# Optimization experiments

Measured on AMD Instinct MI355X. Metric: run time of the kernel, lower is better.

Reference implementation:

```python
import jax, jax.numpy as jnp
import numpy as np

HEAD = 32  # HEAD_SIZE
B, T, C = 8, 1024, 768
LAYER_ID, N_LAYER = 2, 12


def wkv7(r, w, k, v, a, b):
    # RWKV7 linear recurrence (matches the custom CUDA 'attn' kernel math):
    #   S = S * exp(-exp(w)) + (S @ a) b^T + v k^T ;  y = S @ r
    Bb, Tt, Cc = r.shape
    H, N = Cc // HEAD, HEAD
    rs = lambda z: jnp.moveaxis(z.reshape(Bb, Tt, H, N), 1, 0)  # [T,B,H,N]
    rT, kT, vT, aT, bT = rs(r), rs(k), rs(v), rs(a), rs(b)
    wT = rs(jnp.exp(-jnp.exp(w)))  # decay in (0,1)
    def step(S, inp):
        rt, wt, kt, vt, at, bt = inp  # each [B,H,N]
        sa = jnp.einsum('bhij,bhj->bhi', S, at)
        S = S * wt[:, :, None, :] + sa[..., None] * bt[:, :, None, :] + vt[..., None] * kt[:, :, None, :]
        return S, jnp.einsum('bhij,bhj->bhi', S, rt)
    S0 = jnp.zeros((Bb, H, N, N), r.dtype)
    _, y = jax.lax.scan(step, S0, (rT, wT, kT, vT, aT, bT))
    return jnp.moveaxis(y, 0, 1).reshape(Bb, Tt, Cc)


def setup_inputs() -> dict:
    key = jax.random.key(0)
    ks = iter(jax.random.split(key, 64))
    def rn(shape, s=0.02):
        return (jax.random.normal(next(ks), shape, jnp.float32) * s)
    def un(shape, lim):
        return jax.random.uniform(next(ks), shape, jnp.float32, -lim, lim)
    H, N = C // HEAD, HEAD
    r10 = 1.0 - LAYER_ID / N_LAYER          # ratio_1_to_almost0
    r01 = LAYER_ID / (N_LAYER - 1)          # ratio_0_to_1
    ddd = (np.arange(C, dtype=np.float64) / C).reshape(1, 1, C)
    f32 = lambda z: jnp.asarray(z, jnp.float32)
    time_maa_x = f32(1.0 - ddd ** (0.6 * r10 ** 0.9))
    time_maa_rg = f32(1.0 - ddd ** (0.2 * r10))
    time_maa_wa = f32(1.0 - ddd ** (0.9 * r10))
    time_maa_k = f32(1.0 - (ddd ** (0.9 * r10) + 0.4 * r01))
    time_maa_v = f32(1.0 - (ddd ** (0.4 * r10) + 0.6 * r01))
    ds = -7.0 + 5.0 * (np.arange(C, dtype=np.float64) / (C - 1)) ** (0.85 + r01 ** 0.5)
    time_decay = f32(ds.reshape(1, 1, C) + 0.5)
    inp = {
        'x': jax.random.normal(next(ks), (B, T, C), jnp.float32),
        'v1': jax.random.normal(next(ks), (B, T, C), jnp.float32),
        'time_maa_x': time_maa_x, 'time_maa_rg': time_maa_rg, 'time_maa_wa': time_maa_wa,
        'time_maa_k': time_maa_k, 'time_maa_v': time_maa_v,
        'time_decay': time_decay,
        'time_faaaa': rn((1, 1, H, N), 0.05),
        'time_aaaaa': rn((1, 1, C), 0.05),
        'time_maa_w1': rn((C, 28 * 4)), 'time_maa_w2': rn((4, 28, C), 0.05),
        'time_decay_w1': rn((C, 64)), 'time_decay_w2': rn((64, C), 0.05),
        'time_aaa_w1': rn((C, 24)), 'time_aaa_w2': rn((24, C), 0.05),
        'time_kkk_w1': rn((C, 24)), 'time_kkk_w2': rn((24, C), 0.05),
        'gate_w1': rn((C, 120)), 'gate_w2': rn((120, C), 0.05),
        'ma_w1': rn((C, 24)), 'ma_w2': rn((24, C), 0.05), 'time_misc_a': rn((1, 1, C), 0.05),
        'mk_w1': rn((C, 24)), 'mk_w2': rn((24, C), 0.05), 'time_misc_k': rn((1, 1, C), 0.05),
        'mv_w1': rn((C, 24)), 'mv_w2': rn((24, C), 0.05), 'time_misc_v': 1.0 + rn((1, 1, C), 0.05),
        'Wr': un((C, C), 0.5 / C ** 0.5), 'Wk': un((C, C), 0.05 / C ** 0.5),
        'Wv': un((C, C), 0.5 / C ** 0.5), 'Wo': rn((C, C), 0.02),
        'ln_w': jnp.ones((C,), jnp.float32), 'ln_b': jnp.zeros((C,), jnp.float32),
    }
    return inp


def reference(x, v1, time_maa_x, time_maa_rg, time_maa_wa, time_maa_k, time_maa_v,
              time_decay, time_faaaa, time_aaaaa, time_maa_w1, time_maa_w2,
              time_decay_w1, time_decay_w2, time_aaa_w1, time_aaa_w2,
              time_kkk_w1, time_kkk_w2, gate_w1, gate_w2, ma_w1, ma_w2, time_misc_a,
              mk_w1, mk_w2, time_misc_k, mv_w1, mv_w2, time_misc_v,
              Wr, Wk, Wv, Wo, ln_w, ln_b):
    Bb, Tt, Cc = x.shape
    H, N = Cc // HEAD, HEAD
    # token shift: xx[t] = x[t-1] - x[t], with x[-1] = 0
    xsh = jnp.concatenate([jnp.zeros_like(x[:, :1]), x[:, :-1]], axis=1)
    xx = xsh - x
    xxx = x + xx * time_maa_x
    tm = jnp.tanh(xxx @ time_maa_w1).reshape(Bb, Tt, 4, -1)      # [B,T,4,28]
    mix = jnp.einsum('btfd,fdc->fbtc', tm, time_maa_w2)          # [4,B,T,C]
    xrg = x + xx * (time_maa_rg + mix[0])
    xwa = x + xx * (time_maa_wa + mix[1])
    xk = x + xx * (time_maa_k + mix[2])
    xv = x + xx * (time_maa_v + mix[3])
    r = xrg @ Wr
    w = -jax.nn.softplus(-(time_decay + jnp.tanh(xwa @ time_decay_w1) @ time_decay_w2)) - 0.5
    k = xk @ Wk
    v = xv @ Wv
    v = v + (v1 - v) * jax.nn.sigmoid(time_misc_v + xv @ mv_w1 @ mv_w2)
    g = jax.nn.sigmoid(xrg @ gate_w1) @ gate_w2
    kk = k + jnp.tanh(xk @ time_kkk_w1) @ time_kkk_w2
    kk4 = kk.reshape(Bb, Tt, H, N)
    nrm = jnp.maximum(jnp.sqrt(jnp.sum(kk4 * kk4, axis=-1, keepdims=True)), 1e-12)
    kk = (kk4 / nrm).reshape(Bb, Tt, Cc)
    a = jax.nn.sigmoid(time_aaaaa + xwa @ time_aaa_w1 @ time_aaa_w2)
    ma = jax.nn.sigmoid(time_misc_a + xwa @ ma_w1 @ ma_w2)
    k = k * ma + k * a * (1.0 - ma)
    mk = jax.nn.sigmoid(time_misc_k + xk @ mk_w1 @ mk_w2)
    k = k * jnp.exp(jnp.minimum(w * mk, 0.0))
    y = wkv7(r, w, k, v, -kk, kk * a)
    # GroupNorm(n_head groups) over each token, eps=6.4e-5
    yg = y.reshape(Bb, Tt, H, N)
    mu = jnp.mean(yg, axis=-1, keepdims=True)
    var = jnp.var(yg, axis=-1, keepdims=True)
    yn = (yg - mu) * jax.lax.rsqrt(var + 6.4e-05)
    yn = yn * ln_w.reshape(H, N) + ln_b.reshape(H, N)
    # per-head bonus term
    bonus = (jnp.sum(r.reshape(Bb, Tt, H, N) * k.reshape(Bb, Tt, H, N) * time_faaaa,
                     axis=-1, keepdims=True) * v.reshape(Bb, Tt, H, N))
    y = yn.reshape(Bb, Tt, Cc) + bonus.reshape(Bb, Tt, Cc)
    out = (y * g) @ Wo
    return (out, v1)
```

## Files before the change

kernel.cpp:

```cpp
#include <hip/hip_runtime.h>
#include <hip/hip_bf16.h>
#include <math.h>

#define Bdim 8
#define Tdim 1024
#define Cdim 768
#define Hdim 24
#define Ndim 32
#define BTdim (Bdim*Tdim)

typedef __attribute__((ext_vector_type(8))) short bf16x8;
typedef __attribute__((ext_vector_type(4))) float f32x4;
typedef __hip_bfloat16 bf16;

__device__ __forceinline__ float sigm(float x){ return 1.f/(1.f+expf(-x)); }
__device__ __forceinline__ float softplusf(float x){ return fmaxf(x,0.f) + log1pf(expf(-fabsf(x))); }
__device__ __forceinline__ float bf2f(bf16 v){ return __bfloat162float(v); }
__device__ __forceinline__ float us2f(unsigned short s){ return __builtin_bit_cast(float, (unsigned)s<<16); }

template<int CTRL>
__device__ __forceinline__ float dpp_add(float x){
  int xi = __builtin_bit_cast(int, x);
  int yi = __builtin_amdgcn_mov_dpp(xi, CTRL, 0xF, 0xF, true);
  return x + __builtin_bit_cast(float, yi);
}
__device__ __forceinline__ float red32(float x){
  x = dpp_add<0xB1>(x);
  x = dpp_add<0x4E>(x);
  x = dpp_add<0x141>(x);
  x = dpp_add<0x140>(x);
  x += __shfl_xor(x, 16);
  return x;
}
__device__ __forceinline__ float red16(float x){
  x = dpp_add<0xB1>(x);
  x = dpp_add<0x4E>(x);
  x = dpp_add<0x141>(x);
  x = dpp_add<0x140>(x);
  return x;
}

#define GLDS16(gp, lp) __builtin_amdgcn_global_load_lds((const __attribute__((address_space(1))) void*)(gp), (__attribute__((address_space(3))) void*)(lp), 16, 0, 0)

__global__ void k1_shift(const float* __restrict__ x, const float* __restrict__ maa_x,
                         float* __restrict__ xx, bf16* __restrict__ xxx) {
  int idx = blockIdx.x*256 + threadIdx.x;
  if (idx >= BTdim*Cdim) return;
  int c = idx % Cdim; int row = idx / Cdim; int t = row % Tdim;
  float xv = x[idx];
  float xp = (t==0) ? 0.f : x[idx - Cdim];
  float d = xp - xv;
  xx[idx] = d;
  xxx[idx] = __float2bfloat16(xv + d*maa_x[c]);
}

__global__ __launch_bounds__(256) void kconvW(const float* __restrict__ W0, const float* __restrict__ W1,
    const float* __restrict__ W2, const float* __restrict__ W3,
    bf16* __restrict__ T0, bf16* __restrict__ T1, bf16* __restrict__ T2, bf16* __restrict__ T3) {
  const float* Wsrc[4] = {W0,W1,W2,W3};
  bf16* Tdst[4] = {T0,T1,T2,T3};
  const float* W = Wsrc[blockIdx.z];
  bf16* T = Tdst[blockIdx.z];
  __shared__ float tile[32][33];
  int bx = blockIdx.x*32, by = blockIdx.y*32;
  int tx = threadIdx.x & 31, ty = threadIdx.x >> 5;
  #pragma unroll
  for (int q=0;q<32;q+=8) tile[ty+q][tx] = W[(size_t)(by+ty+q)*Cdim + bx+tx];
  __syncthreads();
  #pragma unroll
  for (int q=0;q<32;q+=8) T[(size_t)(bx+ty+q)*Cdim + by+tx] = __float2bfloat16(tile[tx][ty+q]);
}

__global__ __launch_bounds__(256) void kprep(const float* __restrict__ dw1, const float* __restrict__ aaa_w1,
    const float* __restrict__ ma_w1, const float* __restrict__ kkk_w1, const float* __restrict__ mk_w1,
    const float* __restrict__ mv_w1, const float* __restrict__ gate_w1, const float* __restrict__ maa_w1,
    const float* __restrict__ dw2, const float* __restrict__ aaa_w2, const float* __restrict__ ma_w2,
    const float* __restrict__ kkk_w2, const float* __restrict__ mk_w2, const float* __restrict__ mv_w2,
    const float* __restrict__ gate_w2,
    bf16* __restrict__ PWwa, bf16* __restrict__ PWk, bf16* __restrict__ PWv,
    bf16* __restrict__ PWrg, bf16* __restrict__ PWmaa,
    bf16* __restrict__ W2wa, bf16* __restrict__ W2k, bf16* __restrict__ W2v, bf16* __restrict__ W2g){
  int idx = blockIdx.x*256 + threadIdx.x;
  if (idx < 491520) {
    int buf = idx / 98304, rem = idx - buf*98304;
    int n = rem / 768, kk = rem - n*768;
    float val = 0.f;
    bf16* dst;
    switch(buf){
      case 0: dst=PWwa; if(n<64) val=dw1[(size_t)kk*64+n]; else if(n<88) val=aaa_w1[(size_t)kk*24+(n-64)]; else if(n<112) val=ma_w1[(size_t)kk*24+(n-88)]; break;
      case 1: dst=PWk;  if(n<24) val=kkk_w1[(size_t)kk*24+n]; else if(n<48) val=mk_w1[(size_t)kk*24+(n-24)]; break;
      case 2: dst=PWv;  if(n<24) val=mv_w1[(size_t)kk*24+n]; break;
      case 3: dst=PWrg; if(n<120) val=gate_w1[(size_t)kk*120+n]; break;
      default: dst=PWmaa; if(n<112) val=maa_w1[(size_t)kk*112+n]; break;
    }
    dst[rem] = __float2bfloat16(val);
    return;
  }
  int i = idx - 491520;
  if (i < 294912){
    int n=i>>7, q=i&127, seg=n/768, c=n-seg*768;
    float val=0.f;
    if (seg==0){ if(q<64) val=dw2[(size_t)q*768+c]; }
    else if (seg==1){ if(q>=64&&q<88) val=aaa_w2[(size_t)(q-64)*768+c]; }
    else { if(q>=88&&q<112) val=ma_w2[(size_t)(q-88)*768+c]; }
    W2wa[i]=__float2bfloat16(val); return;
  }
  i -= 294912;
  if (i < 98304){
    int n=i>>6, q=i&63, seg=n/768, c=n-seg*768;
    float val=0.f;
    if (seg==0){ if(q<24) val=kkk_w2[(size_t)q*768+c]; }
    else { if(q>=24&&q<48) val=mk_w2[(size_t)(q-24)*768+c]; }
    W2k[i]=__float2bfloat16(val); return;
  }
  i -= 98304;
  if (i < 24576){
    int c=i>>5, q=i&31;
    float val = (q<24) ? mv_w2[(size_t)q*768+c] : 0.f;
    W2v[i]=__float2bfloat16(val); return;
  }
  i -= 24576;
  if (i < 98304){
    int c=i>>7, q=i&127;
    float val = (q<120) ? gate_w2[(size_t)q*768+c] : 0.f;
    W2g[i]=__float2bfloat16(val);
  }
}

__global__ __launch_bounds__(256) void gemm_mfma(const bf16* __restrict__ A,
    const bf16* __restrict__ Bt, float* __restrict__ C, int M, int N, int K) {
  __shared__ unsigned short As[128*32];
  __shared__ unsigned short Bs[128*32];
  const int bm = blockIdx.y*128, bn = blockIdx.x*128;
  const int tid = threadIdx.x, lane = tid&63, w = tid>>6;
  const int wr = w>>1, wc = w&1;
  const int lr = lane&15, kg = lane>>4;
  f32x4 zero = {0.f,0.f,0.f,0.f};
  f32x4 acc[4][4];
  #pragma unroll
  for (int m=0;m<4;m++)
    #pragma unroll
    for (int n=0;n<4;n++) acc[m][n]=zero;
  const size_t rowA = (size_t)(bm + w*32 + (lane>>2))*K + (lane&3)*8;
  const size_t rowB = (size_t)(bn + w*32 + (lane>>2))*K + (lane&3)*8;
  unsigned short* lA = As + w*32*32;
  unsigned short* lB = Bs + w*32*32;
  for (int k0=0; k0<K; k0+=32){
    GLDS16(A + rowA + k0,                 lA);
    GLDS16(A + rowA + k0 + (size_t)16*K,  lA + 512);
    GLDS16(Bt + rowB + k0,                lB);
    GLDS16(Bt + rowB + k0 + (size_t)16*K, lB + 512);
    __syncthreads();
    bf16x8 af[4], bfr[4];
    #pragma unroll
    for (int m=0;m<4;m++) af[m]  = *(const bf16x8*)(void*)(As + (wr*64+m*16+lr)*32 + kg*8);
    #pragma unroll
    for (int n=0;n<4;n++) bfr[n] = *(const bf16x8*)(void*)(Bs + (wc*64+n*16+lr)*32 + kg*8);
    #pragma unroll
    for (int m=0;m<4;m++)
      #pragma unroll
      for (int n=0;n<4;n++)
        acc[m][n] = __builtin_amdgcn_mfma_f32_16x16x32_bf16(af[m], bfr[n], acc[m][n], 0,0,0);
    __syncthreads();
  }
  #pragma unroll
  for (int m=0;m<4;m++)
    #pragma unroll
    for (int n=0;n<4;n++){
      size_t r0 = (size_t)(bm + wr*64 + m*16 + kg*4);
      int cc = bn + wc*64 + n*16 + lr;
      #pragma unroll
      for (int q=0;q<4;q++)
        C[(r0+q)*N + cc] = acc[m][n][q];
    }
}

struct G3 {
  const bf16* A[3];
  const bf16* Bt[3];
  bf16* C[3];
};
__global__ __launch_bounds__(256) void gemm_big3(G3 p, int N, int K) {
  const int z = blockIdx.z;
  const bf16* __restrict__ A  = p.A[z];
  const bf16* __restrict__ Bt = p.Bt[z];
  bf16* __restrict__ C = p.C[z];
  __shared__ unsigned short As[128*32];
  __shared__ unsigned short Bs[128*32];
  const int bm = blockIdx.y*128, bn = blockIdx.x*128;
  const int tid = threadIdx.x, lane = tid&63, w = tid>>6;
  const int wr = w>>1, wc = w&1;
  const int lr = lane&15, kg = lane>>4;
  f32x4 zero = {0.f,0.f,0.f,0.f};
  f32x4 acc[4][4];
  #pragma unroll
  for (int m=0;m<4;m++)
    #pragma unroll
    for (int n=0;n<4;n++) acc[m][n]=zero;
  const size_t rowA = (size_t)(bm + w*32 + (lane>>2))*K + (lane&3)*8;
  const size_t rowB = (size_t)(bn + w*32 + (lane>>2))*K + (lane&3)*8;
  unsigned short* lA = As + w*32*32;
  unsigned short* lB = Bs + w*32*32;
  for (int k0=0; k0<K; k0+=32){
    GLDS16(A + rowA + k0,                 lA);
    GLDS16(A + rowA + k0 + (size_t)16*K,  lA + 512);
    GLDS16(Bt + rowB + k0,                lB);
    GLDS16(Bt + rowB + k0 + (size_t)16*K, lB + 512);
    __syncthreads();
    bf16x8 af[4], bfr[4];
    #pragma unroll
    for (int m=0;m<4;m++) af[m]  = *(const bf16x8*)(void*)(As + (wr*64+m*16+lr)*32 + kg*8);
    #pragma unroll
    for (int n=0;n<4;n++) bfr[n] = *(const bf16x8*)(void*)(Bs + (wc*64+n*16+lr)*32 + kg*8);
    #pragma unroll
    for (int m=0;m<4;m++)
      #pragma unroll
      for (int n=0;n<4;n++)
        acc[m][n] = __builtin_amdgcn_mfma_f32_16x16x32_bf16(af[m], bfr[n], acc[m][n], 0,0,0);
    __syncthreads();
  }
  #pragma unroll
  for (int m=0;m<4;m++)
    #pragma unroll
    for (int n=0;n<4;n++){
      size_t r0 = (size_t)(bm + wr*64 + m*16 + kg*4);
      int cc = bn + wc*64 + n*16 + lr;
      #pragma unroll
      for (int q=0;q<4;q++)
        C[(r0+q)*N + cc] = __float2bfloat16(acc[m][n][q]);
    }
}

__global__ __launch_bounds__(256) void gemm_tm(const bf16* __restrict__ A,
    const bf16* __restrict__ Bt, float* __restrict__ C, int K) {
  __shared__ unsigned short As[128*32];
  __shared__ unsigned short Bs[128*32];
  const int bm = blockIdx.y*128;
  const int tid = threadIdx.x, lane = tid&63, w = tid>>6;
  const int wr = w>>1, wc = w&1;
  const int lr = lane&15, kg = lane>>4;
  f32x4 zero = {0.f,0.f,0.f,0.f};
  f32x4 acc[4][4];
  #pragma unroll
  for (int m=0;m<4;m++)
    #pragma unroll
    for (int n=0;n<4;n++) acc[m][n]=zero;
  const size_t rowA = (size_t)(bm + w*32 + (lane>>2))*K + (lane&3)*8;
  const size_t rowB = (size_t)(w*32 + (lane>>2))*K + (lane&3)*8;
  unsigned short* lA = As + w*32*32;
  unsigned short* lB = Bs + w*32*32;
  for (int k0=0; k0<K; k0+=32){
    GLDS16(A + rowA + k0,                 lA);
    GLDS16(A + rowA + k0 + (size_t)16*K,  lA + 512);
    GLDS16(Bt + rowB + k0,                lB);
    GLDS16(Bt + rowB + k0 + (size_t)16*K, lB + 512);
    __syncthreads();
    bf16x8 af[4], bfr[4];
    #pragma unroll
    for (int m=0;m<4;m++) af[m]  = *(const bf16x8*)(void*)(As + (wr*64+m*16+lr)*32 + kg*8);
    #pragma unroll
    for (int n=0;n<4;n++) bfr[n] = *(const bf16x8*)(void*)(Bs + (wc*64+n*16+lr)*32 + kg*8);
    #pragma unroll
    for (int m=0;m<4;m++)
      #pragma unroll
      for (int n=0;n<4;n++)
        acc[m][n] = __builtin_amdgcn_mfma_f32_16x16x32_bf16(af[m], bfr[n], acc[m][n], 0,0,0);
    __syncthreads();
  }
  #pragma unroll
  for (int m=0;m<4;m++)
    #pragma unroll
    for (int n=0;n<4;n++){
      size_t r0 = (size_t)(bm + wr*64 + m*16 + kg*4);
      int cc = wc*64 + n*16 + lr;
      if (cc < 112){
        #pragma unroll
        for (int q=0;q<4;q++)
          C[(r0+q)*112 + cc] = tanhf(acc[m][n][q]);
      }
    }
}

struct S1P {
  const bf16* A[4];
  const bf16* Bt[4];
  bf16* C[4];
  int Ntrue[4];
  int Nalloc[4];
  int act[4];
};
__global__ __launch_bounds__(256) void gemm_s1(S1P p, int K) {
  const int z = blockIdx.z;
  const bf16* __restrict__ A  = p.A[z];
  const bf16* __restrict__ Bt = p.Bt[z];
  bf16* __restrict__ C = p.C[z];
  const int Ntrue = p.Ntrue[z], Nalloc = p.Nalloc[z], act = p.act[z];
  __shared__ unsigned short As[128*32];
  __shared__ unsigned short Bs[128*32];
  const int bm = blockIdx.y*128;
  const int tid = threadIdx.x, lane = tid&63, w = tid>>6;
  const int wr = w>>1, wc = w&1;
  const int lr = lane&15, kg = lane>>4;
  f32x4 zero = {0.f,0.f,0.f,0.f};
  f32x4 acc[4][4];
  #pragma unroll
  for (int m=0;m<4;m++)
    #pragma unroll
    for (int n=0;n<4;n++) acc[m][n]=zero;
  const size_t rowA = (size_t)(bm + w*32 + (lane>>2))*K + (lane&3)*8;
  const size_t rowB = (size_t)(w*32 + (lane>>2))*K + (lane&3)*8;
  unsigned short* lA = As + w*32*32;
  unsigned short* lB = Bs + w*32*32;
  for (int k0=0; k0<K; k0+=32){
    GLDS16(A + rowA + k0,                 lA);
    GLDS16(A + rowA + k0 + (size_t)16*K,  lA + 512);
    GLDS16(Bt + rowB + k0,                lB);
    GLDS16(Bt + rowB + k0 + (size_t)16*K, lB + 512);
    __syncthreads();
    bf16x8 af[4], bfr[4];
    #pragma unroll
    for (int m=0;m<4;m++) af[m]  = *(const bf16x8*)(void*)(As + (wr*64+m*16+lr)*32 + kg*8);
    #pragma unroll
    for (int n=0;n<4;n++) bfr[n] = *(const bf16x8*)(void*)(Bs + (wc*64+n*16+lr)*32 + kg*8);
    #pragma unroll
    for (int m=0;m<4;m++)
      #pragma unroll
      for (int n=0;n<4;n++)
        acc[m][n] = __builtin_amdgcn_mfma_f32_16x16x32_bf16(af[m], bfr[n], acc[m][n], 0,0,0);
    __syncthreads();
  }
  #pragma unroll
  for (int m=0;m<4;m++)
    #pragma unroll
    for (int n=0;n<4;n++){
      size_t r0 = (size_t)(bm + wr*64 + m*16 + kg*4);
      int cc = wc*64 + n*16 + lr;
      if (cc < Nalloc){
        #pragma unroll
        for (int q=0;q<4;q++){
          float val = acc[m][n][q];
          if      (act==1){ if (cc<64) val = tanhf(val); }
          else if (act==2){ if (cc<24) val = tanhf(val); }
          else if (act==3){ val = sigm(val); }
          if (cc >= Ntrue) val = 0.f;
          C[(r0+q)*Nalloc + cc] = __float2bfloat16(val);
        }
      }
    }
}

struct Z4 {
  const bf16* A[4];
  const bf16* Bt[4];
  bf16* C[4];
  int N[4];
  int K[4];
};
__global__ __launch_bounds__(256) void gemm_z(Z4 p) {
  const int z = blockIdx.z;
  const int N = p.N[z], K = p.K[z];
  const int bn = blockIdx.x*128;
  if (bn >= N) return;
  const bf16* __restrict__ A  = p.A[z];
  const bf16* __restrict__ Bt = p.Bt[z];
  bf16* __restrict__ C = p.C[z];
  __shared__ unsigned short As[128*32];
  __shared__ unsigned short Bs[128*32];
  const int bm = blockIdx.y*128;
  const int tid = threadIdx.x, lane = tid&63, w = tid>>6;
  const int wr = w>>1, wc = w&1;
  const int lr = lane&15, kg = lane>>4;
  f32x4 zero = {0.f,0.f,0.f,0.f};
  f32x4 acc[4][4];
  #pragma unroll
  for (int m=0;m<4;m++)
    #pragma unroll
    for (int n=0;n<4;n++) acc[m][n]=zero;
  const size_t rowA = (size_t)(bm + w*32 + (lane>>2))*K + (lane&3)*8;
  const size_t rowB = (size_t)(bn + w*32 + (lane>>2))*K + (lane&3)*8;
  unsigned short* lA = As + w*32*32;
  unsigned short* lB = Bs + w*32*32;
  for (int k0=0; k0<K; k0+=32){
    GLDS16(A + rowA + k0,                 lA);
    GLDS16(A + rowA + k0 + (size_t)16*K,  lA + 512);
    GLDS16(Bt + rowB + k0,                lB);
    GLDS16(Bt + rowB + k0 + (size_t)16*K, lB + 512);
    __syncthreads();
    bf16x8 af[4], bfr[4];
    #pragma unroll
    for (int m=0;m<4;m++) af[m]  = *(const bf16x8*)(void*)(As + (wr*64+m*16+lr)*32 + kg*8);
    #pragma unroll
    for (int n=0;n<4;n++) bfr[n] = *(const bf16x8*)(void*)(Bs + (wc*64+n*16+lr)*32 + kg*8);
    #pragma unroll
    for (int m=0;m<4;m++)
      #pragma unroll
      for (int n=0;n<4;n++)
        acc[m][n] = __builtin_amdgcn_mfma_f32_16x16x32_bf16(af[m], bfr[n], acc[m][n], 0,0,0);
    __syncthreads();
  }
  #pragma unroll
  for (int m=0;m<4;m++)
    #pragma unroll
    for (int n=0;n<4;n++){
      size_t r0 = (size_t)(bm + wr*64 + m*16 + kg*4);
      int cc = bn + wc*64 + n*16 + lr;
      #pragma unroll
      for (int q=0;q<4;q++)
        C[(r0+q)*N + cc] = __float2bfloat16(acc[m][n][q]);
    }
}

__global__ __launch_bounds__(256) void k2_mix(const float* __restrict__ x, const float* __restrict__ xx,
    const float* __restrict__ tm, const float* __restrict__ w2,
    const float* __restrict__ mrg, const float* __restrict__ mwa,
    const float* __restrict__ mk_, const float* __restrict__ mv_,
    bf16* __restrict__ xrg, bf16* __restrict__ xwa, bf16* __restrict__ xk, bf16* __restrict__ xv) {
  const int row0 = blockIdx.x*8, tid = threadIdx.x;
  __shared__ float stm[8][112];
  for (int idx=tid; idx<8*112; idx+=256){
    int rr=idx/112, q=idx-rr*112;
    stm[rr][q]=tm[(size_t)(row0+rr)*112+q];
  }
  __syncthreads();
  for (int c=tid;c<Cdim;c+=256){
    float x8[8], d8[8];
    #pragma unroll
    for (int rr=0;rr<8;rr++){
      size_t i=(size_t)(row0+rr)*Cdim+c;
      x8[rr]=x[i]; d8[rr]=xx[i];
    }
    float mrgc=mrg[c], mwac=mwa[c], mkc=mk_[c], mvc=mv_[c];
    float m0[8]={},m1[8]={},m2[8]={},m3[8]={};
    #pragma unroll 4
    for (int d=0; d<28; d++){
      float w0=w2[(size_t)(d)*Cdim + c];
      float w1=w2[(size_t)(28+d)*Cdim + c];
      float w2v=w2[(size_t)(56+d)*Cdim + c];
      float w3=w2[(size_t)(84+d)*Cdim + c];
      #pragma unroll
      for (int rr=0;rr<8;rr++){
        m0[rr]+=stm[rr][d]*w0; m1[rr]+=stm[rr][28+d]*w1;
        m2[rr]+=stm[rr][56+d]*w2v; m3[rr]+=stm[rr][84+d]*w3;
      }
    }
    #pragma unroll
    for (int rr=0;rr<8;rr++){
      size_t i=(size_t)(row0+rr)*Cdim+c;
      xrg[i]=__float2bfloat16(x8[rr] + d8[rr]*(mrgc+m0[rr]));
      xwa[i]=__float2bfloat16(x8[rr] + d8[rr]*(mwac+m1[rr]));
      xk[i] =__float2bfloat16(x8[rr] + d8[rr]*(mkc+m2[rr]));
      xv[i] =__float2bfloat16(x8[rr] + d8[rr]*(mvc+m3[rr]));
    }
  }
}

__global__ __launch_bounds__(256) void k5_fuse(
    const bf16* __restrict__ zwa, const bf16* __restrict__ zk, const bf16* __restrict__ zv,
    const bf16* __restrict__ rbf, const bf16* __restrict__ kbf, bf16* __restrict__ vbf,
    const float* __restrict__ td, const float* __restrict__ aaaaa,
    const float* __restrict__ misc_a, const float* __restrict__ misc_k, const float* __restrict__ misc_v,
    const float* __restrict__ v1,
    float* __restrict__ wexp, unsigned short* __restrict__ rkab) {
  const int row = blockIdx.x, tid = threadIdx.x;
  #pragma unroll
  for (int it=0;it<3;it++){
    const int c = tid + it*256;
    const size_t i = (size_t)row*Cdim + c;
    float kraw = bf2f(kbf[i]);
    float v0   = bf2f(vbf[i]);
    float zd = bf2f(zwa[(size_t)row*2304 + c]);
    float za = bf2f(zwa[(size_t)row*2304 + 768 + c]);
    float zma= bf2f(zwa[(size_t)row*2304 + 1536 + c]);
    float zkk= bf2f(zk[(size_t)row*1536 + c]);
    float zmk= bf2f(zk[(size_t)row*1536 + 768 + c]);
    float zmv= bf2f(zv[i]);
    float w = -softplusf(-(td[c]+zd)) - 0.5f;
    wexp[i] = expf(-expf(w));
    float a  = sigm(aaaaa[c]+za);
    float ma = sigm(misc_a[c]+zma);
    float mk = sigm(misc_k[c]+zmk);
    float mv = sigm(misc_v[c]+zmv);
    vbf[i] = __float2bfloat16(v0 + (v1[i]-v0)*mv);
    float kf = kraw*(ma + a*(1.f-ma))*expf(fminf(w*mk,0.f));
    float kk = kraw + zkk;
    float ss = red32(kk*kk);
    float kkn = kk * (1.f/fmaxf(sqrtf(ss),1e-12f));
    unsigned rus = (unsigned)__builtin_bit_cast(unsigned short, rbf[i]);
    unsigned kus = (unsigned)__builtin_bit_cast(unsigned short, __float2bfloat16(kf));
    unsigned aus = (unsigned)__builtin_bit_cast(unsigned short, __float2bfloat16(-kkn));
    unsigned bus = (unsigned)__builtin_bit_cast(unsigned short, __float2bfloat16(kkn*a));
    uint2 pk;
    pk.x = rus | (kus<<16);
    pk.y = aus | (bus<<16);
    *(uint2*)&rkab[((size_t)row*Hdim + (c>>5))*128 + (size_t)(c&31)*4] = pk;
  }
}

__global__ __launch_bounds__(64) void k6_wkv(const unsigned short* __restrict__ rkab,
    const float* __restrict__ wd, const unsigned short* __restrict__ vbf, bf16* __restrict__ y) {
  const int lane = threadIdx.x;
  const int bid = blockIdx.x;
  const int head = bid % (Bdim*Hdim);
  const int rq   = bid / (Bdim*Hdim);
  const int bb = head / Hdim, hh = head - bb*Hdim;
  const int i0 = rq*4 + (lane >> 4);
  const int jh = lane & 15;
  __shared__ __align__(16) unsigned short srk[2][16][128];
  __shared__ __align__(16) float sw[2][16][32];
  __shared__ __align__(16) unsigned short sv[2][16][32];
  const size_t wvbase = (size_t)bb*Tdim*Cdim + (size_t)hh*Ndim;
  float S0=0.f, S1=0.f;

  auto rkrow = [&](size_t t){ return (((size_t)bb*Tdim + t)*Hdim + hh)*128; };
  auto STAGE = [&](int c, int buf){
    const size_t tb = (size_t)c*16;
    #pragma unroll
    for (int i=0;i<4;i++)
      GLDS16(rkab + rkrow(tb + i*4 + (lane>>4)) + (size_t)(lane&15)*8, &srk[buf][i*4][0]);
    GLDS16(wd + wvbase + (tb +     (lane>>3))*Cdim + (lane&7)*4, &sw[buf][0][0]);
    GLDS16(wd + wvbase + (tb + 8 + (lane>>3))*Cdim + (lane&7)*4, &sw[buf][8][0]);
    GLDS16(vbf + wvbase + (tb + (lane>>2))*Cdim + (lane&3)*8, &sv[buf][0][0]);
  };

  uint4 nq; float2 nw; unsigned short nv;
  auto LOADT = [&](int buf, int t){
    nq = *(const uint4*)&srk[buf][t][jh*8];
    nw = *(const float2*)&sw[buf][t][jh*2];
    nv = sv[buf][t][i0];
  };

  STAGE(0, 0);
  asm volatile("s_waitcnt vmcnt(0)" ::: "memory");
  LOADT(0, 0);
  int buf = 0;
  const int NCH = Tdim/16;
  for (int c=0; c<NCH; ++c){
    if (c+1 < NCH) STAGE(c+1, buf^1);
    const size_t yb = wvbase + (size_t)c*16*Cdim;
    #pragma unroll
    for (int t=0; t<16; t++){
      const uint4 q = nq;
      const float2 cw = nw;
      const unsigned short cv = nv;
      if (t < 15) {
        LOADT(buf, t+1);
      } else if (c+1 < NCH) {
        asm volatile("s_waitcnt vmcnt(0)" ::: "memory");
        LOADT(buf^1, 0);
      }
      float r0 = __builtin_bit_cast(float, q.x<<16);
      float k0 = __builtin_bit_cast(float, q.x & 0xFFFF0000u);
      float a0 = __builtin_bit_cast(float, q.y<<16);
      float b0 = __builtin_bit_cast(float, q.y & 0xFFFF0000u);
      float r1 = __builtin_bit_cast(float, q.z<<16);
      float k1 = __builtin_bit_cast(float, q.z & 0xFFFF0000u);
      float a1 = __builtin_bit_cast(float, q.w<<16);
      float b1 = __builtin_bit_cast(float, q.w & 0xFFFF0000u);
      const float vl = us2f(cv);
      float sa = S0*a0 + S1*a1;
      sa = red16(sa);
      S0 = S0*cw.x + (sa*b0 + vl*k0);
      S1 = S1*cw.y + (sa*b1 + vl*k1);
      float yv = S0*r0 + S1*r1;
      yv = red16(yv);
      if (jh == 0) y[yb + (size_t)t*Cdim + i0] = __float2bfloat16(yv);
    }
    buf ^= 1;
  }
}

__global__ __launch_bounds__(256) void k7_post(const bf16* __restrict__ y,
    const unsigned short* __restrict__ rkab, const bf16* __restrict__ v,
    const bf16* __restrict__ g, const float* __restrict__ faaaa,
    const float* __restrict__ lnw, const float* __restrict__ lnb,
    bf16* __restrict__ ygate,
    const float4* __restrict__ v1c, float4* __restrict__ outc) {
  const int row = blockIdx.x, tid = threadIdx.x;
  if (tid < 192) outc[(size_t)row*192 + tid] = v1c[(size_t)row*192 + tid];
  #pragma unroll
  for (int it=0; it<3; it++){
    const int c = tid + it*256;
    const size_t i = (size_t)row*Cdim + c;
    float yv = bf2f(y[i]);
    unsigned rk = *(const unsigned*)&rkab[((size_t)row*Hdim + (c>>5))*128 + (size_t)(c&31)*4];
    float rf = __builtin_bit_cast(float, rk<<16);
    float kf = __builtin_bit_cast(float, rk & 0xFFFF0000u);
    float bon = rf*kf*faaaa[c];
    float s  = red32(yv);
    float ss = red32(yv*yv);
    float bn = red32(bon);
    float mu = s*(1.f/Ndim);
    float var = ss*(1.f/Ndim) - mu*mu;
    float rs = rsqrtf(var + 6.4e-5f);
    float yn = (yv-mu)*rs*lnw[c]+lnb[c];
    ygate[i]=__float2bfloat16((yn + bn*bf2f(v[i]))*bf2f(g[i]));
  }
}

extern "C" void kernel_launch(void* const* d_in, const int* in_sizes, int n_in,
                              void* d_out, int out_size, void* d_ws, size_t ws_size,
                              hipStream_t stream) {
  const float* x      = (const float*)d_in[0];
  const float* v1     = (const float*)d_in[1];
  const float* maa_x  = (const float*)d_in[2];
  const float* maa_rg = (const float*)d_in[3];
  const float* maa_wa = (const float*)d_in[4];
  const float* maa_k  = (const float*)d_in[5];
  const float* maa_v  = (const float*)d_in[6];
  const float* time_decay = (const float*)d_in[7];
  const float* faaaa  = (const float*)d_in[8];
  const float* aaaaa  = (const float*)d_in[9];
  const float* maa_w1 = (const float*)d_in[10];
  const float* maa_w2 = (const float*)d_in[11];
  const float* dw1    = (const float*)d_in[12];
  const float* dw2    = (const float*)d_in[13];
  const float* aaa_w1 = (const float*)d_in[14];
  const float* aaa_w2 = (const float*)d_in[15];
  const float* kkk_w1 = (const float*)d_in[16];
  const float* kkk_w2 = (const float*)d_in[17];
  const float* gate_w1= (const float*)d_in[18];
  const float* gate_w2= (const float*)d_in[19];
  const float* ma_w1  = (const float*)d_in[20];
  const float* ma_w2  = (const float*)d_in[21];
  const float* misc_a = (const float*)d_in[22];
  const float* mk_w1  = (const float*)d_in[23];
  const float* mk_w2  = (const float*)d_in[24];
  const float* misc_k = (const float*)d_in[25];
  const float* mv_w1  = (const float*)d_in[26];
  const float* mv_w2  = (const float*)d_in[27];
  const float* misc_v = (const float*)d_in[28];
  const float* Wr     = (const float*)d_in[29];
  const float* Wk     = (const float*)d_in[30];
  const float* Wv     = (const float*)d_in[31];
  const float* Wo     = (const float*)d_in[32];
  const float* lnw    = (const float*)d_in[33];
  const float* lnb    = (const float*)d_in[34];
  float* out = (float*)d_out;

  float* ws = (float*)d_ws;
  const size_t BTC = (size_t)BTdim*Cdim;
  const size_t HB  = BTC/2;
  float* xx    = ws;
  float* wexp  = ws;
  bf16* kb_bf  = (bf16*)(ws + 2*HB);
  bf16* ybuf_bf= (bf16*)(ws + 2*HB);
  bf16* vb_bf  = (bf16*)(ws + 3*HB);
  bf16* xrg_bf = (bf16*)(ws + 4*HB);
  bf16* xwa_bf = xrg_bf + BTC;
  bf16* zwa_bf = (bf16*)(ws + 4*HB);
  bf16* xk_bf  = (bf16*)(ws + 7*HB);
  bf16* xv_bf  = xk_bf + BTC;
  bf16* zk_bf  = (bf16*)(ws + 7*HB);
  bf16* xxx_bf = (bf16*)(ws + 9*HB);
  bf16* zv_bf  = (bf16*)(ws + 9*HB);
  float* tm    = ws + 10*HB;
  bf16* zg_bf  = (bf16*)(ws + 10*HB);
  bf16* hwa_bf = (bf16*)(ws + 11*HB);
  bf16* hk_bf  = hwa_bf + (size_t)BTdim*128;
  bf16* hv_bf  = hk_bf  + (size_t)BTdim*64;
  bf16* hrg_bf = hv_bf  + (size_t)BTdim*32;
  unsigned short* rkab = (unsigned short*)(ws + 12*HB);
  bf16* rb_bf  = (bf16*)(ws + 16*HB);
  bf16* yg_bf  = (bf16*)(ws + 17*HB);
  bf16* Wbase  = (bf16*)(ws + 18*HB);
  bf16* WtR = Wbase;
  bf16* WtK = WtR + 589824;
  bf16* WtV = WtK + 589824;
  bf16* WtO = WtV + 589824;
  bf16* PWwa = WtO + 589824;
  bf16* PWk  = PWwa + 98304;
  bf16* PWv  = PWk  + 98304;
  bf16* PWrg = PWv  + 98304;
  bf16* PWmaa= PWrg + 98304;
  bf16* W2wa = PWmaa + 98304;
  bf16* W2k  = W2wa + 294912;
  bf16* W2v  = W2k  + 98304;
  bf16* W2g  = W2v  + 24576;

  dim3 blk(256);
  kconvW<<<dim3(24,24,4), blk, 0, stream>>>(Wr,Wk,Wv,Wo, WtR,WtK,WtV,WtO);
  kprep<<<dim3(3936), blk, 0, stream>>>(dw1,aaa_w1,ma_w1,kkk_w1,mk_w1,mv_w1,gate_w1,maa_w1,
                                        dw2,aaa_w2,ma_w2,kkk_w2,mk_w2,mv_w2,gate_w2,
                                        PWwa,PWk,PWv,PWrg,PWmaa, W2wa,W2k,W2v,W2g);
  k1_shift<<<dim3((BTdim*Cdim+255)/256), blk, 0, stream>>>(x, maa_x, xx, xxx_bf);
  gemm_tm<<<dim3(1,64), blk, 0, stream>>>(xxx_bf, PWmaa, tm, Cdim);
  k2_mix<<<dim3(BTdim/8), blk, 0, stream>>>(x, xx, tm, maa_w2, maa_rg, maa_wa, maa_k, maa_v,
                                            xrg_bf, xwa_bf, xk_bf, xv_bf);
  {
    S1P p{};
    p.A[0]=xwa_bf; p.Bt[0]=PWwa; p.C[0]=hwa_bf; p.Ntrue[0]=112; p.Nalloc[0]=128; p.act[0]=1;
    p.A[1]=xk_bf;  p.Bt[1]=PWk;  p.C[1]=hk_bf;  p.Ntrue[1]=48;  p.Nalloc[1]=64;  p.act[1]=2;
    p.A[2]=xv_bf;  p.Bt[2]=PWv;  p.C[2]=hv_bf;  p.Ntrue[2]=24;  p.Nalloc[2]=32;  p.act[2]=0;
    p.A[3]=xrg_bf; p.Bt[3]=PWrg; p.C[3]=hrg_bf; p.Ntrue[3]=120; p.Nalloc[3]=128; p.act[3]=3;
    gemm_s1<<<dim3(1,64,4), blk, 0, stream>>>(p, Cdim);
  }
  {
    G3 p{};
    p.A[0]=xrg_bf; p.Bt[0]=WtR; p.C[0]=rb_bf;
    p.A[1]=xk_bf;  p.Bt[1]=WtK; p.C[1]=kb_bf;
    p.A[2]=xv_bf;  p.Bt[2]=WtV; p.C[2]=vb_bf;
    gemm_big3<<<dim3(6,64,3), blk, 0, stream>>>(p, Cdim, Cdim);
  }
  {
    Z4 p{};
    p.A[0]=hwa_bf; p.Bt[0]=W2wa; p.C[0]=zwa_bf; p.N[0]=2304; p.K[0]=128;
    p.A[1]=hk_bf;  p.Bt[1]=W2k;  p.C[1]=zk_bf;  p.N[1]=1536; p.K[1]=64;
    p.A[2]=hv_bf;  p.Bt[2]=W2v;  p.C[2]=zv_bf;  p.N[2]=768;  p.K[2]=32;
    p.A[3]=hrg_bf; p.Bt[3]=W2g;  p.C[3]=zg_bf;  p.N[3]=768;  p.K[3]=128;
    gemm_z<<<dim3(18,64,4), blk, 0, stream>>>(p);
  }
  k5_fuse<<<dim3(BTdim), blk, 0, stream>>>(zwa_bf, zk_bf, zv_bf, rb_bf, kb_bf, vb_bf,
      time_decay, aaaaa, misc_a, misc_k, misc_v, v1, wexp, rkab);
  k6_wkv<<<dim3(Bdim*Hdim*8), dim3(64), 0, stream>>>(rkab, wexp,
      (const unsigned short*)vb_bf, ybuf_bf);
  k7_post<<<dim3(BTdim), blk, 0, stream>>>(ybuf_bf, rkab, vb_bf, zg_bf, faaaa, lnw, lnb, yg_bf,
                                           (const float4*)v1, (float4*)(out + BTC));
  gemm_mfma<<<dim3(6,64), blk, 0, stream>>>(yg_bf, WtO, out, BTdim, Cdim, Cdim);
}
```

Measured before the change: 523.6 us.

## Fuse weight prep kernels, merge small and big GEMMs, drop xx buffer, retile Wo GEMM

Merges the weight transpose and the weight prep kernels into one launch. It also merges the low-rank first-stage GEMM and the three big R/K/V GEMMs into a single launch with a block-index dispatch. The time-shift difference is now recomputed inside k2_mix instead of being written to and read back from a full fp32 xx buffer. The output GEMM uses 64-row tiles, which doubles the block count to fill more CUs. These changes cut launch overhead and memory traffic, at the cost of a fused kernel that mixes heterogeneous block workloads and an extra read of x in k2_mix.

```diff
diff --git a/kernel.cpp b/kernel.cpp
--- a/kernel.cpp
+++ b/kernel.cpp
@@ -43,35 +43,19 @@
 #define GLDS16(gp, lp) __builtin_amdgcn_global_load_lds((const __attribute__((address_space(1))) void*)(gp), (__attribute__((address_space(3))) void*)(lp), 16, 0, 0)
 
 __global__ void k1_shift(const float* __restrict__ x, const float* __restrict__ maa_x,
-                         float* __restrict__ xx, bf16* __restrict__ xxx) {
+                         bf16* __restrict__ xxx) {
   int idx = blockIdx.x*256 + threadIdx.x;
   if (idx >= BTdim*Cdim) return;
   int c = idx % Cdim; int row = idx / Cdim; int t = row % Tdim;
   float xv = x[idx];
   float xp = (t==0) ? 0.f : x[idx - Cdim];
-  float d = xp - xv;
-  xx[idx] = d;
-  xxx[idx] = __float2bfloat16(xv + d*maa_x[c]);
-}
-
-__global__ __launch_bounds__(256) void kconvW(const float* __restrict__ W0, const float* __restrict__ W1,
+  xxx[idx] = __float2bfloat16(xv + (xp - xv)*maa_x[c]);
+}
+
+__global__ __launch_bounds__(256) void kcp(const float* __restrict__ W0, const float* __restrict__ W1,
     const float* __restrict__ W2, const float* __restrict__ W3,
-    bf16* __restrict__ T0, bf16* __restrict__ T1, bf16* __restrict__ T2, bf16* __restrict__ T3) {
-  const float* Wsrc[4] = {W0,W1,W2,W3};
-  bf16* Tdst[4] = {T0,T1,T2,T3};
-  const float* W = Wsrc[blockIdx.z];
-  bf16* T = Tdst[blockIdx.z];
-  __shared__ float tile[32][33];
-  int bx = blockIdx.x*32, by = blockIdx.y*32;
-  int tx = threadIdx.x & 31, ty = threadIdx.x >> 5;
-  #pragma unroll
-  for (int q=0;q<32;q+=8) tile[ty+q][tx] = W[(size_t)(by+ty+q)*Cdim + bx+tx];
-  __syncthreads();
-  #pragma unroll
-  for (int q=0;q<32;q+=8) T[(size_t)(bx+ty+q)*Cdim + by+tx] = __float2bfloat16(tile[tx][ty+q]);
-}
-
-__global__ __launch_bounds__(256) void kprep(const float* __restrict__ dw1, const float* __restrict__ aaa_w1,
+    bf16* __restrict__ T0, bf16* __restrict__ T1, bf16* __restrict__ T2, bf16* __restrict__ T3,
+    const float* __restrict__ dw1, const float* __restrict__ aaa_w1,
     const float* __restrict__ ma_w1, const float* __restrict__ kkk_w1, const float* __restrict__ mk_w1,
     const float* __restrict__ mv_w1, const float* __restrict__ gate_w1, const float* __restrict__ maa_w1,
     const float* __restrict__ dw2, const float* __restrict__ aaa_w2, const float* __restrict__ ma_w2,
@@ -80,7 +64,24 @@
     bf16* __restrict__ PWwa, bf16* __restrict__ PWk, bf16* __restrict__ PWv,
     bf16* __restrict__ PWrg, bf16* __restrict__ PWmaa,
     bf16* __restrict__ W2wa, bf16* __restrict__ W2k, bf16* __restrict__ W2v, bf16* __restrict__ W2g){
-  int idx = blockIdx.x*256 + threadIdx.x;
+  const int bid = blockIdx.x;
+  if (bid < 2304) {
+    __shared__ float tile[32][33];
+    const int z = bid/576, rem = bid - z*576;
+    const int by = (rem/24)*32, bx = (rem%24)*32;
+    const float* Wsrc[4] = {W0,W1,W2,W3};
+    bf16* Tdst[4] = {T0,T1,T2,T3};
+    const float* W = Wsrc[z];
+    bf16* T = Tdst[z];
+    int tx = threadIdx.x & 31, ty = threadIdx.x >> 5;
+    #pragma unroll
+    for (int q=0;q<32;q+=8) tile[ty+q][tx] = W[(size_t)(by+ty+q)*Cdim + bx+tx];
+    __syncthreads();
+    #pragma unroll
+    for (int q=0;q<32;q+=8) T[(size_t)(bx+ty+q)*Cdim + by+tx] = __float2bfloat16(tile[tx][ty+q]);
+    return;
+  }
+  int idx = (bid-2304)*256 + threadIdx.x;
   if (idx < 491520) {
     int buf = idx / 98304, rem = idx - buf*98304;
     int n = rem / 768, kk = rem - n*768;
@@ -127,14 +128,134 @@
   }
 }
 
-__global__ __launch_bounds__(256) void gemm_mfma(const bf16* __restrict__ A,
-    const bf16* __restrict__ Bt, float* __restrict__ C, int M, int N, int K) {
-  __shared__ unsigned short As[128*32];
+__global__ __launch_bounds__(256) void gemm_wo(const bf16* __restrict__ A,
+    const bf16* __restrict__ Bt, float* __restrict__ C, int N, int K) {
+  __shared__ unsigned short As[64*32];
   __shared__ unsigned short Bs[128*32];
-  const int bm = blockIdx.y*128, bn = blockIdx.x*128;
+  const int bm = blockIdx.y*64, bn = blockIdx.x*128;
   const int tid = threadIdx.x, lane = tid&63, w = tid>>6;
   const int wr = w>>1, wc = w&1;
   const int lr = lane&15, kg = lane>>4;
+  f32x4 zero = {0.f,0.f,0.f,0.f};
+  f32x4 acc[2][4];
+  #pragma unroll
+  for (int m=0;m<2;m++)
+    #pragma unroll
+    for (int n=0;n<4;n++) acc[m][n]=zero;
+  const size_t rowA = (size_t)(bm + w*16 + (lane>>2))*K + (lane&3)*8;
+  const size_t rowB = (size_t)(bn + w*32 + (lane>>2))*K + (lane&3)*8;
+  unsigned short* lA = As + w*16*32;
+  unsigned short* lB = Bs + w*32*32;
+  for (int k0=0; k0<K; k0+=32){
+    GLDS16(A + rowA + k0,                 lA);
+    GLDS16(Bt + rowB + k0,                lB);
+    GLDS16(Bt + rowB + k0 + (size_t)16*K, lB + 512);
+    __syncthreads();
+    bf16x8 af[2], bfr[4];
+    #pragma unroll
+    for (int m=0;m<2;m++) af[m]  = *(const bf16x8*)(void*)(As + (wr*32+m*16+lr)*32 + kg*8);
+    #pragma unroll
+    for (int n=0;n<4;n++) bfr[n] = *(const bf16x8*)(void*)(Bs + (wc*64+n*16+lr)*32 + kg*8);
+    #pragma unroll
+    for (int m=0;m<2;m++)
+      #pragma unroll
+      for (int n=0;n<4;n++)
+        acc[m][n] = __builtin_amdgcn_mfma_f32_16x16x32_bf16(af[m], bfr[n], acc[m][n], 0,0,0);
+    __syncthreads();
+  }
+  #pragma unroll
+  for (int m=0;m<2;m++)
+    #pragma unroll
+    for (int n=0;n<4;n++){
+      size_t r0 = (size_t)(bm + wr*32 + m*16 + kg*4);
+      int cc = bn + wc*64 + n*16 + lr;
+      #pragma unroll
+      for (int q=0;q<4;q++)
+        C[(r0+q)*N + cc] = acc[m][n][q];
+    }
+}
+
+__global__ __launch_bounds__(256) void gemm_tm(const bf16* __restrict__ A,
+    const bf16* __restrict__ Bt, float* __restrict__ C, int K) {
+  __shared__ unsigned short As[128*32];
+  __shared__ unsigned short Bs[128*32];
+  const int bm = blockIdx.y*128;
+  const int tid = threadIdx.x, lane = tid&63, w = tid>>6;
+  const int wr = w>>1, wc = w&1;
+  const int lr = lane&15, kg = lane>>4;
+  f32x4 zero = {0.f,0.f,0.f,0.f};
+  f32x4 acc[4][4];
+  #pragma unroll
+  for (int m=0;m<4;m++)
+    #pragma unroll
+    for (int n=0;n<4;n++) acc[m][n]=zero;
+  const size_t rowA = (size_t)(bm + w*32 + (lane>>2))*K + (lane&3)*8;
+  const size_t rowB = (size_t)(w*32 + (lane>>2))*K + (lane&3)*8;
+  unsigned short* lA = As + w*32*32;
+  unsigned short* lB = Bs + w*32*32;
+  for (int k0=0; k0<K; k0+=32){
+    GLDS16(A + rowA + k0,                 lA);
+    GLDS16(A + rowA + k0 + (size_t)16*K,  lA + 512);
+    GLDS16(Bt + rowB + k0,                lB);
+    GLDS16(Bt + rowB + k0 + (size_t)16*K, lB + 512);
+    __syncthreads();
+    bf16x8 af[4], bfr[4];
+    #pragma unroll
+    for (int m=0;m<4;m++) af[m]  = *(const bf16x8*)(void*)(As + (wr*64+m*16+lr)*32 + kg*8);
+    #pragma unroll
+    for (int n=0;n<4;n++) bfr[n] = *(const bf16x8*)(void*)(Bs + (wc*64+n*16+lr)*32 + kg*8);
+    #pragma unroll
+    for (int m=0;m<4;m++)
+      #pragma unroll
+      for (int n=0;n<4;n++)
+        acc[m][n] = __builtin_amdgcn_mfma_f32_16x16x32_bf16(af[m], bfr[n], acc[m][n], 0,0,0);
+    __syncthreads();
+  }
+  #pragma unroll
+  for (int m=0;m<4;m++)
+    #pragma unroll
+    for (int n=0;n<4;n++){
+      size_t r0 = (size_t)(bm + wr*64 + m*16 + kg*4);
+      int cc = wc*64 + n*16 + lr;
+      if (cc < 112){
+        #pragma unroll
+        for (int q=0;q<4;q++)
+          C[(r0+q)*112 + cc] = tanhf(acc[m][n][q]);
+      }
+    }
+}
+
+struct S1P {
+  const bf16* A[4];
+  const bf16* Bt[4];
+  bf16* C[4];
+  int Ntrue[4];
+  int Nalloc[4];
+  int act[4];
+};
+struct G3 {
+  const bf16* A[3];
+  const bf16* Bt[3];
+  bf16* C[3];
+};
+__global__ __launch_bounds__(256) void gemm_s1b3(S1P s, G3 g, int K) {
+  const int bid = blockIdx.x;
+  __shared__ unsigned short As[128*32];
+  __shared__ unsigned short Bs[128*32];
+  const int tid = threadIdx.x, lane = tid&63, w = tid>>6;
+  const int wr = w>>1, wc = w&1;
+  const int lr = lane&15, kg = lane>>4;
+  int bm, bn, z;
+  const bf16 *A, *Bt;
+  const bool small = (bid < 256);
+  if (small){
+    z = bid>>6; bm = (bid&63)*128; bn = 0;
+    A = s.A[z]; Bt = s.Bt[z];
+  } else {
+    int rem = bid-256; z = rem/384; int r2 = rem - z*384;
+    bm = (r2/6)*128; bn = (r2%6)*128;
+    A = g.A[z]; Bt = g.Bt[z];
+  }
   f32x4 zero = {0.f,0.f,0.f,0.f};
   f32x4 acc[4][4];
   #pragma unroll
@@ -163,190 +284,40 @@
         acc[m][n] = __builtin_amdgcn_mfma_f32_16x16x32_bf16(af[m], bfr[n], acc[m][n], 0,0,0);
     __syncthreads();
   }
-  #pragma unroll
-  for (int m=0;m<4;m++)
-    #pragma unroll
-    for (int n=0;n<4;n++){
-      size_t r0 = (size_t)(bm + wr*64 + m*16 + kg*4);
-      int cc = bn + wc*64 + n*16 + lr;
-      #pragma unroll
-      for (int q=0;q<4;q++)
-        C[(r0+q)*N + cc] = acc[m][n][q];
-    }
-}
-
-struct G3 {
-  const bf16* A[3];
-  const bf16* Bt[3];
-  bf16* C[3];
-};
-__global__ __launch_bounds__(256) void gemm_big3(G3 p, int N, int K) {
-  const int z = blockIdx.z;
-  const bf16* __restrict__ A  = p.A[z];
-  const bf16* __restrict__ Bt = p.Bt[z];
-  bf16* __restrict__ C = p.C[z];
-  __shared__ unsigned short As[128*32];
-  __shared__ unsigned short Bs[128*32];
-  const int bm = blockIdx.y*128, bn = blockIdx.x*128;
-  const int tid = threadIdx.x, lane = tid&63, w = tid>>6;
-  const int wr = w>>1, wc = w&1;
-  const int lr = lane&15, kg = lane>>4;
-  f32x4 zero = {0.f,0.f,0.f,0.f};
-  f32x4 acc[4][4];
-  #pragma unroll
-  for (int m=0;m<4;m++)
-    #pragma unroll
-    for (int n=0;n<4;n++) acc[m][n]=zero;
-  const size_t rowA = (size_t)(bm + w*32 + (lane>>2))*K + (lane&3)*8;
-  const size_t rowB = (size_t)(bn + w*32 + (lane>>2))*K + (lane&3)*8;
-  unsigned short* lA = As + w*32*32;
-  unsigned short* lB = Bs + w*32*32;
-  for (int k0=0; k0<K; k0+=32){
-    GLDS16(A + rowA + k0,                 lA);
-    GLDS16(A + rowA + k0 + (size_t)16*K,  lA + 512);
-    GLDS16(Bt + rowB + k0,                lB);
-    GLDS16(Bt + rowB + k0 + (size_t)16*K, lB + 512);
-    __syncthreads();
-    bf16x8 af[4], bfr[4];
-    #pragma unroll
-    for (int m=0;m<4;m++) af[m]  = *(const bf16x8*)(void*)(As + (wr*64+m*16+lr)*32 + kg*8);
-    #pragma unroll
-    for (int n=0;n<4;n++) bfr[n] = *(const bf16x8*)(void*)(Bs + (wc*64+n*16+lr)*32 + kg*8);
+  if (small){
+    bf16* __restrict__ C = s.C[z];
+    const int Ntrue = s.Ntrue[z], Nalloc = s.Nalloc[z], act = s.act[z];
     #pragma unroll
     for (int m=0;m<4;m++)
       #pragma unroll
-      for (int n=0;n<4;n++)
-        acc[m][n] = __builtin_amdgcn_mfma_f32_16x16x32_bf16(af[m], bfr[n], acc[m][n], 0,0,0);
-    __syncthreads();
-  }
-  #pragma unroll
-  for (int m=0;m<4;m++)
-    #pragma unroll
-    for (int n=0;n<4;n++){
-      size_t r0 = (size_t)(bm + wr*64 + m*16 + kg*4);
-      int cc = bn + wc*64 + n*16 + lr;
-      #pragma unroll
-      for (int q=0;q<4;q++)
-        C[(r0+q)*N + cc] = __float2bfloat16(acc[m][n][q]);
-    }
-}
-
-__global__ __launch_bounds__(256) void gemm_tm(const bf16* __restrict__ A,
-    const bf16* __restrict__ Bt, float* __restrict__ C, int K) {
-  __shared__ unsigned short As[128*32];
-  __shared__ unsigned short Bs[128*32];
-  const int bm = blockIdx.y*128;
-  const int tid = threadIdx.x, lane = tid&63, w = tid>>6;
-  const int wr = w>>1, wc = w&1;
-  const int lr = lane&15, kg = lane>>4;
-  f32x4 zero = {0.f,0.f,0.f,0.f};
-  f32x4 acc[4][4];
-  #pragma unroll
-  for (int m=0;m<4;m++)
-    #pragma unroll
-    for (int n=0;n<4;n++) acc[m][n]=zero;
-  const size_t rowA = (size_t)(bm + w*32 + (lane>>2))*K + (lane&3)*8;
-  const size_t rowB = (size_t)(w*32 + (lane>>2))*K + (lane&3)*8;
-  unsigned short* lA = As + w*32*32;
-  unsigned short* lB = Bs + w*32*32;
-  for (int k0=0; k0<K; k0+=32){
-    GLDS16(A + rowA + k0,                 lA);
-    GLDS16(A + rowA + k0 + (size_t)16*K,  lA + 512);
-    GLDS16(Bt + rowB + k0,                lB);
-    GLDS16(Bt + rowB + k0 + (size_t)16*K, lB + 512);
-    __syncthreads();
-    bf16x8 af[4], bfr[4];
-    #pragma unroll
-    for (int m=0;m<4;m++) af[m]  = *(const bf16x8*)(void*)(As + (wr*64+m*16+lr)*32 + kg*8);
-    #pragma unroll
-    for (int n=0;n<4;n++) bfr[n] = *(const bf16x8*)(void*)(Bs + (wc*64+n*16+lr)*32 + kg*8);
+      for (int n=0;n<4;n++){
+        size_t r0 = (size_t)(bm + wr*64 + m*16 + kg*4);
+        int cc = wc*64 + n*16 + lr;
+        if (cc < Nalloc){
+          #pragma unroll
+          for (int q=0;q<4;q++){
+            float val = acc[m][n][q];
+            if      (act==1){ if (cc<64) val = tanhf(val); }
+            else if (act==2){ if (cc<24) val = tanhf(val); }
+            else if (act==3){ val = sigm(val); }
+            if (cc >= Ntrue) val = 0.f;
+            C[(r0+q)*Nalloc + cc] = __float2bfloat16(val);
+          }
+        }
+      }
+  } else {
+    bf16* __restrict__ C = g.C[z];
     #pragma unroll
     for (int m=0;m<4;m++)
       #pragma unroll
-      for (int n=0;n<4;n++)
-        acc[m][n] = __builtin_amdgcn_mfma_f32_16x16x32_bf16(af[m], bfr[n], acc[m][n], 0,0,0);
-    __syncthreads();
-  }
-  #pragma unroll
-  for (int m=0;m<4;m++)
-    #pragma unroll
-    for (int n=0;n<4;n++){
-      size_t r0 = (size_t)(bm + wr*64 + m*16 + kg*4);
-      int cc = wc*64 + n*16 + lr;
-      if (cc < 112){
+      for (int n=0;n<4;n++){
+        size_t r0 = (size_t)(bm + wr*64 + m*16 + kg*4);
+        int cc = bn + wc*64 + n*16 + lr;
         #pragma unroll
         for (int q=0;q<4;q++)
-          C[(r0+q)*112 + cc] = tanhf(acc[m][n][q]);
+          C[(r0+q)*Cdim + cc] = __float2bfloat16(acc[m][n][q]);
       }
-    }
-}
-
-struct S1P {
-  const bf16* A[4];
-  const bf16* Bt[4];
-  bf16* C[4];
-  int Ntrue[4];
-  int Nalloc[4];
-  int act[4];
-};
-__global__ __launch_bounds__(256) void gemm_s1(S1P p, int K) {
-  const int z = blockIdx.z;
-  const bf16* __restrict__ A  = p.A[z];
-  const bf16* __restrict__ Bt = p.Bt[z];
-  bf16* __restrict__ C = p.C[z];
-  const int Ntrue = p.Ntrue[z], Nalloc = p.Nalloc[z], act = p.act[z];
-  __shared__ unsigned short As[128*32];
-  __shared__ unsigned short Bs[128*32];
-  const int bm = blockIdx.y*128;
-  const int tid = threadIdx.x, lane = tid&63, w = tid>>6;
-  const int wr = w>>1, wc = w&1;
-  const int lr = lane&15, kg = lane>>4;
-  f32x4 zero = {0.f,0.f,0.f,0.f};
-  f32x4 acc[4][4];
-  #pragma unroll
-  for (int m=0;m<4;m++)
-    #pragma unroll
-    for (int n=0;n<4;n++) acc[m][n]=zero;
-  const size_t rowA = (size_t)(bm + w*32 + (lane>>2))*K + (lane&3)*8;
-  const size_t rowB = (size_t)(w*32 + (lane>>2))*K + (lane&3)*8;
-  unsigned short* lA = As + w*32*32;
-  unsigned short* lB = Bs + w*32*32;
-  for (int k0=0; k0<K; k0+=32){
-    GLDS16(A + rowA + k0,                 lA);
-    GLDS16(A + rowA + k0 + (size_t)16*K,  lA + 512);
-    GLDS16(Bt + rowB + k0,                lB);
-    GLDS16(Bt + rowB + k0 + (size_t)16*K, lB + 512);
-    __syncthreads();
-    bf16x8 af[4], bfr[4];
-    #pragma unroll
-    for (int m=0;m<4;m++) af[m]  = *(const bf16x8*)(void*)(As + (wr*64+m*16+lr)*32 + kg*8);
-    #pragma unroll
-    for (int n=0;n<4;n++) bfr[n] = *(const bf16x8*)(void*)(Bs + (wc*64+n*16+lr)*32 + kg*8);
-    #pragma unroll
-    for (int m=0;m<4;m++)
-      #pragma unroll
-      for (int n=0;n<4;n++)
-        acc[m][n] = __builtin_amdgcn_mfma_f32_16x16x32_bf16(af[m], bfr[n], acc[m][n], 0,0,0);
-    __syncthreads();
-  }
-  #pragma unroll
-  for (int m=0;m<4;m++)
-    #pragma unroll
-    for (int n=0;n<4;n++){
-      size_t r0 = (size_t)(bm + wr*64 + m*16 + kg*4);
-      int cc = wc*64 + n*16 + lr;
-      if (cc < Nalloc){
-        #pragma unroll
-        for (int q=0;q<4;q++){
-          float val = acc[m][n][q];
-          if      (act==1){ if (cc<64) val = tanhf(val); }
-          else if (act==2){ if (cc<24) val = tanhf(val); }
-          else if (act==3){ val = sigm(val); }
-          if (cc >= Ntrue) val = 0.f;
-          C[(r0+q)*Nalloc + cc] = __float2bfloat16(val);
-        }
-      }
-    }
+  }
 }
 
 struct Z4 {
@@ -410,7 +381,7 @@
     }
 }
 
-__global__ __launch_bounds__(256) void k2_mix(const float* __restrict__ x, const float* __restrict__ xx,
+__global__ __launch_bounds__(256) void k2_mix(const float* __restrict__ x,
     const float* __restrict__ tm, const float* __restrict__ w2,
     const float* __restrict__ mrg, const float* __restrict__ mwa,
     const float* __restrict__ mk_, const float* __restrict__ mv_,
@@ -427,7 +398,9 @@
     #pragma unroll
     for (int rr=0;rr<8;rr++){
       size_t i=(size_t)(row0+rr)*Cdim+c;
-      x8[rr]=x[i]; d8[rr]=xx[i];
+      float xv = x[i];
+      float xp = (((row0+rr) & (Tdim-1)) == 0) ? 0.f : x[i - Cdim];
+      x8[rr]=xv; d8[rr]=xp - xv;
     }
     float mrgc=mrg[c], mwac=mwa[c], mkc=mk_[c], mvc=mv_[c];
     float m0[8]={},m1[8]={},m2[8]={},m3[8]={};
@@ -640,7 +613,6 @@
   float* ws = (float*)d_ws;
   const size_t BTC = (size_t)BTdim*Cdim;
   const size_t HB  = BTC/2;
-  float* xx    = ws;
   float* wexp  = ws;
   bf16* kb_bf  = (bf16*)(ws + 2*HB);
   bf16* ybuf_bf= (bf16*)(ws + 2*HB);
@@ -678,28 +650,25 @@
   bf16* W2g  = W2v  + 24576;
 
   dim3 blk(256);
-  kconvW<<<dim3(24,24,4), blk, 0, stream>>>(Wr,Wk,Wv,Wo, WtR,WtK,WtV,WtO);
-  kprep<<<dim3(3936), blk, 0, stream>>>(dw1,aaa_w1,ma_w1,kkk_w1,mk_w1,mv_w1,gate_w1,maa_w1,
-                                        dw2,aaa_w2,ma_w2,kkk_w2,mk_w2,mv_w2,gate_w2,
-                                        PWwa,PWk,PWv,PWrg,PWmaa, W2wa,W2k,W2v,W2g);
-  k1_shift<<<dim3((BTdim*Cdim+255)/256), blk, 0, stream>>>(x, maa_x, xx, xxx_bf);
+  k1_shift<<<dim3((BTdim*Cdim+255)/256), blk, 0, stream>>>(x, maa_x, xxx_bf);
+  kcp<<<dim3(2304+3936), blk, 0, stream>>>(Wr,Wk,Wv,Wo, WtR,WtK,WtV,WtO,
+                                           dw1,aaa_w1,ma_w1,kkk_w1,mk_w1,mv_w1,gate_w1,maa_w1,
+                                           dw2,aaa_w2,ma_w2,kkk_w2,mk_w2,mv_w2,gate_w2,
+                                           PWwa,PWk,PWv,PWrg,PWmaa, W2wa,W2k,W2v,W2g);
   gemm_tm<<<dim3(1,64), blk, 0, stream>>>(xxx_bf, PWmaa, tm, Cdim);
-  k2_mix<<<dim3(BTdim/8), blk, 0, stream>>>(x, xx, tm, maa_w2, maa_rg, maa_wa, maa_k, maa_v,
+  k2_mix<<<dim3(BTdim/8), blk, 0, stream>>>(x, tm, maa_w2, maa_rg, maa_wa, maa_k, maa_v,
                                             xrg_bf, xwa_bf, xk_bf, xv_bf);
   {
-    S1P p{};
-    p.A[0]=xwa_bf; p.Bt[0]=PWwa; p.C[0]=hwa_bf; p.Ntrue[0]=112; p.Nalloc[0]=128; p.act[0]=1;
-    p.A[1]=xk_bf;  p.Bt[1]=PWk;  p.C[1]=hk_bf;  p.Ntrue[1]=48;  p.Nalloc[1]=64;  p.act[1]=2;
-    p.A[2]=xv_bf;  p.Bt[2]=PWv;  p.C[2]=hv_bf;  p.Ntrue[2]=24;  p.Nalloc[2]=32;  p.act[2]=0;
-    p.A[3]=xrg_bf; p.Bt[3]=PWrg; p.C[3]=hrg_bf; p.Ntrue[3]=120; p.Nalloc[3]=128; p.act[3]=3;
-    gemm_s1<<<dim3(1,64,4), blk, 0, stream>>>(p, Cdim);
-  }
-  {
-    G3 p{};
-    p.A[0]=xrg_bf; p.Bt[0]=WtR; p.C[0]=rb_bf;
-    p.A[1]=xk_bf;  p.Bt[1]=WtK; p.C[1]=kb_bf;
-    p.A[2]=xv_bf;  p.Bt[2]=WtV; p.C[2]=vb_bf;
-    gemm_big3<<<dim3(6,64,3), blk, 0, stream>>>(p, Cdim, Cdim);
+    S1P s{};
+    s.A[0]=xwa_bf; s.Bt[0]=PWwa; s.C[0]=hwa_bf; s.Ntrue[0]=112; s.Nalloc[0]=128; s.act[0]=1;
+    s.A[1]=xk_bf;  s.Bt[1]=PWk;  s.C[1]=hk_bf;  s.Ntrue[1]=48;  s.Nalloc[1]=64;  s.act[1]=2;
+    s.A[2]=xv_bf;  s.Bt[2]=PWv;  s.C[2]=hv_bf;  s.Ntrue[2]=24;  s.Nalloc[2]=32;  s.act[2]=0;
+    s.A[3]=xrg_bf; s.Bt[3]=PWrg; s.C[3]=hrg_bf; s.Ntrue[3]=120; s.Nalloc[3]=128; s.act[3]=3;
+    G3 g{};
+    g.A[0]=xrg_bf; g.Bt[0]=WtR; g.C[0]=rb_bf;
+    g.A[1]=xk_bf;  g.Bt[1]=WtK; g.C[1]=kb_bf;
+    g.A[2]=xv_bf;  g.Bt[2]=WtV; g.C[2]=vb_bf;
+    gemm_s1b3<<<dim3(256 + 3*384), blk, 0, stream>>>(s, g, Cdim);
   }
   {
     Z4 p{};
@@ -715,5 +684,5 @@
       (const unsigned short*)vb_bf, ybuf_bf);
   k7_post<<<dim3(BTdim), blk, 0, stream>>>(ybuf_bf, rkab, vb_bf, zg_bf, faaaa, lnw, lnb, yg_bf,
                                            (const float4*)v1, (float4*)(out + BTC));
-  gemm_mfma<<<dim3(6,64), blk, 0, stream>>>(yg_bf, WtO, out, BTdim, Cdim, Cdim);
-}
+  gemm_wo<<<dim3(6,128), blk, 0, stream>>>(yg_bf, WtO, out, Cdim, Cdim);
+}
```

Measured after the change: 516.9 us. Within noise of the previous version (-1.3%).
